# Performance work log

Measured on AMD Instinct MI355X. Metric: run time of the kernel, lower is better.

The kernel has to match this reference:

```python
import jax, jax.numpy as jnp
import numpy as np
from itertools import permutations

B, L, H, A, E, R, BS = 4, 1024, 768, 12, 32, 97, 64
P = E * (E - 1)  # ordered entity pairs per sample
HTS = np.array(list(permutations(range(E), 2)), dtype=np.int32)  # [P,2]


def setup_inputs() -> dict:
    key = jax.random.key(0)
    ks = jax.random.split(key, 8)
    return {
        "hidden_state": jax.random.normal(ks[0], (B, L, H), jnp.float32),
        "attention": jax.random.uniform(ks[1], (B, A, L, L), jnp.float32),
        "attention_mask": jnp.ones((B, L), jnp.float32),
        "head": jax.random.randint(ks[2], (B, E), 0, L, jnp.int32),
        "tail": jax.random.randint(ks[3], (B, E), 0, L, jnp.int32),
        # params (stored [in, out])
        "Wh": jax.random.normal(ks[4], (2 * H, H), jnp.float32) * 0.02,
        "bh": jnp.zeros((H,), jnp.float32),
        "Wt": jax.random.normal(ks[5], (2 * H, H), jnp.float32) * 0.02,
        "bt": jnp.zeros((H,), jnp.float32),
        "Wc": jax.random.normal(ks[6], (H * BS, R), jnp.float32) * 0.01,
        "bc": jnp.zeros((R,), jnp.float32),
    }


def reference(hidden_state, attention, attention_mask, head, tail, Wh, bh, Wt, bt, Wc, bc):
    attn = attention.mean(axis=1)  # [B,L,L]
    hts0 = jnp.asarray(HTS[:, 0])
    hts1 = jnp.asarray(HTS[:, 1])

    def per_sample(hid, at, hd, tl, am):
        ent_feat = (hid[hd] + hid[tl]) * 0.5   # [E,H]
        ent_attn = (at[hd] + at[tl]) * 0.5     # [E,L]
        head_f = ent_feat[hts0]                # [P,H]
        tail_f = ent_feat[hts1]                # [P,H]
        ht_attn = ent_attn[hts0] * ent_attn[hts1] * am  # [P,L]
        ht_attn = ht_attn / (ht_attn.sum(-1, keepdims=True) + 1e-20)
        ht_info = ht_attn @ hid                # [P,H]
        return (jnp.concatenate([head_f, ht_info], -1),
                jnp.concatenate([tail_f, ht_info], -1))

    all_h, all_t = jax.vmap(per_sample)(hidden_state, attn, head, tail, attention_mask)
    all_h = all_h.reshape(-1, 2 * H)  # [B*P, 2H]
    all_t = all_t.reshape(-1, 2 * H)
    h = jnp.tanh(all_h @ Wh + bh)     # [N,H]
    t = jnp.tanh(all_t @ Wt + bt)
    N = h.shape[0]
    # GroupLinear: block-diagonal outer product then linear
    outer = (h.reshape(N, H // BS, BS, 1) * t.reshape(N, H // BS, 1, BS)).reshape(N, H * BS)
    logits = outer @ Wc + bc          # [N,R]
    return logits
```

## Files before the change

kernel.cpp:

```cpp
#include <hip/hip_runtime.h>
#include <cstdint>
#include <cstddef>

#define BB 4
#define LL 1024
#define HH 768
#define AA 12
#define EE 32
#define PP 992
#define PPAD 1024
#define NROW (BB*PPAD)
#define NN (BB*PP)
#define RR 97
#define RP 112
#define GS2 16

typedef __attribute__((ext_vector_type(8))) _Float16 half8;
typedef __attribute__((ext_vector_type(4))) _Float16 half4v;
typedef __attribute__((ext_vector_type(2))) _Float16 half2v;
typedef __attribute__((ext_vector_type(4))) float floatx4;

union H8u { half8 v8; half2v v2[4]; };

#define WAITVM(N) asm volatile("s_waitcnt vmcnt(" #N ")" ::: "memory")

__device__ __forceinline__ void gl_lds16(const void* g, void* l) {
    __builtin_amdgcn_global_load_lds(
        (const __attribute__((address_space(1))) unsigned int*)g,
        (__attribute__((address_space(3))) unsigned int*)l, 16, 0, 0);
}

__device__ __forceinline__ void barrier_raw() {
    asm volatile("" ::: "memory");
    __builtin_amdgcn_s_barrier();
    __builtin_amdgcn_sched_barrier(0);
    asm volatile("" ::: "memory");
}

__device__ __forceinline__ int xswz96(int bid) {
    return (bid & 7) * 96 + (bid >> 3);
}

__device__ __forceinline__ void pair_decode(int p, int& i0, int& i1) {
    i0 = p / 31;
    int r = p - i0 * 31;
    i1 = r + (r >= i0 ? 1 : 0);
}

__device__ __forceinline__ float fast_tanh(float x) {
    float ax = fabsf(x);
    float t = __builtin_amdgcn_exp2f(ax * -2.885390082f);
    float r = (1.f - t) * __builtin_amdgcn_rcpf(1.f + t);
    return copysignf(r, x);
}

__global__ __launch_bounds__(256) void k_stage0(
        const float* __restrict__ hid, const float* __restrict__ att,
        const int* __restrict__ head, const int* __restrict__ tail,
        const float* __restrict__ Wh, const float* __restrict__ Wt,
        const float* __restrict__ Wc,
        _Float16* __restrict__ hidb, _Float16* __restrict__ Whf,
        _Float16* __restrict__ Wtf, _Float16* __restrict__ Wcp,
        float* __restrict__ ent_feat, float* __restrict__ ent_attn) {
    __shared__ float ldw[32][101];
    int bid = blockIdx.x, tid = threadIdx.x;
    if (bid < 1536) {
        int ksg = bid;
        int w = tid >> 6, lane = tid & 63;
        const float* src = Wc + (size_t)ksg * 32 * RR;
        #pragma unroll
        for (int rr = 0; rr < 8; ++rr) {
            int row = w * 8 + rr;
            ldw[row][lane] = src[(size_t)row * RR + lane];
            if (lane < 33) ldw[row][64 + lane] = src[(size_t)row * RR + 64 + lane];
        }
        __syncthreads();
        #pragma unroll
        for (int j = 0; j < 2; ++j) {
            int f = tid + j * 256;
            int rt = f >> 6, lf = f & 63;
            int c = rt * 16 + (lf & 15);
            int kb = (lf >> 4) * 8;
            _Float16 v[8];
            #pragma unroll
            for (int e = 0; e < 8; ++e)
                v[e] = (c < RR) ? (_Float16)ldw[kb + e][c] : (_Float16)0.f;
            *(half8*)(Wcp + ((size_t)ksg * 512 + f) * 8) = *(const half8*)v;
        }
    } else if (bid < 2112) {
        int which = (bid < 1824) ? 0 : 1;
        const float* src = (which ? Wt : Wh) + (size_t)HH * HH;
        _Float16* dst = which ? Wtf : Whf;
        int idx = (bid - (which ? 1824 : 1536)) * 256 + tid;
        int lane = idx & 63, f = idx >> 6;
        int ct = f % 48, ks = f / 48;
        int c = ct * 16 + (lane & 15);
        int kb = ks * 32 + (lane >> 4) * 8;
        _Float16 v[8];
        #pragma unroll
        for (int e = 0; e < 8; ++e)
            v[e] = (_Float16)src[(size_t)(kb + e) * HH + c];
        *(half8*)(dst + (size_t)idx * 8) = *(const half8*)v;
    } else if (bid < 3648) {
        int idx = (bid - 2112) * 256 + tid;
        const float* s = hid + (size_t)idx * 8;
        float4 a = *(const float4*)s;
        float4 b = *(const float4*)(s + 4);
        half8 v = { (_Float16)a.x, (_Float16)a.y, (_Float16)a.z, (_Float16)a.w,
                    (_Float16)b.x, (_Float16)b.y, (_Float16)b.z, (_Float16)b.w };
        *(half8*)(hidb + (size_t)idx * 8) = v;
    } else {
        int q = bid - 3648;
        int be = q >> 2, qt = q & 3;
        int b = be >> 5;
        int hd = head[be], tl = tail[be];
        const float* hrow = hid + ((size_t)b * LL + hd) * HH;
        const float* trow = hid + ((size_t)b * LL + tl) * HH;
        if (tid < 192) {
            int c = qt * 192 + tid;
            ent_feat[(size_t)be * HH + c] = 0.5f * (hrow[c] + trow[c]);
        }
        const float* abase = att + (size_t)b * AA * LL * LL;
        int ll = qt * 256 + tid;
        float s = 0.f;
        #pragma unroll
        for (int a = 0; a < AA; ++a) {
            const float* ar = abase + (size_t)a * LL * LL;
            s += ar[(size_t)hd * LL + ll] + ar[(size_t)tl * LL + ll];
        }
        ent_attn[(size_t)be * LL + ll] = s * (0.5f / AA);
    }
}

__global__ __launch_bounds__(256) void k_stage1(
        const float* __restrict__ ent_attn, const float* __restrict__ am,
        const float* __restrict__ ent_feat,
        const float* __restrict__ Wh, const float* __restrict__ bh,
        const float* __restrict__ Wt, const float* __restrict__ bt,
        _Float16* __restrict__ pairw, float* __restrict__ Fht) {
    __shared__ float fs[EE][68];
    __shared__ float ws_[64][68];
    int tid = threadIdx.x;
    if (blockIdx.x < 1024) {
        int lane = tid & 63, w = tid >> 6;
        int prow = blockIdx.x * 4 + w;
        int b = prow >> 10, p = prow & 1023;
        _Float16* dst = pairw + (size_t)prow * LL;
        if (p >= PP) {
            #pragma unroll
            for (int c = 0; c < 4; ++c) {
                half4v z = {};
                *(half4v*)(dst + c * 256 + lane * 4) = z;
            }
            return;
        }
        int i0, i1; pair_decode(p, i0, i1);
        const float* e0  = ent_attn + ((size_t)b * EE + i0) * LL;
        const float* e1  = ent_attn + ((size_t)b * EE + i1) * LL;
        const float* amr = am + (size_t)b * LL;
        float wv[16];
        float s = 0.f;
        #pragma unroll
        for (int c = 0; c < 4; ++c) {
            int o = c * 256 + lane * 4;
            float4 a = *(const float4*)(e0 + o);
            float4 d = *(const float4*)(e1 + o);
            float4 m = *(const float4*)(amr + o);
            wv[c*4+0] = a.x * d.x * m.x; wv[c*4+1] = a.y * d.y * m.y;
            wv[c*4+2] = a.z * d.z * m.z; wv[c*4+3] = a.w * d.w * m.w;
            s += wv[c*4+0] + wv[c*4+1] + wv[c*4+2] + wv[c*4+3];
        }
        #pragma unroll
        for (int off = 32; off > 0; off >>= 1) s += __shfl_down(s, off, 64);
        float tot = __shfl(s, 0, 64);
        float inv = 1.0f / (tot + 1e-20f);
        #pragma unroll
        for (int c = 0; c < 4; ++c) {
            half4v o4 = { (_Float16)(wv[c*4+0] * inv), (_Float16)(wv[c*4+1] * inv),
                          (_Float16)(wv[c*4+2] * inv), (_Float16)(wv[c*4+3] * inv) };
            *(half4v*)(dst + c * 256 + lane * 4) = o4;
        }
    } else {
        int q = blockIdx.x - 1024;
        int ct = q % 12, b = (q / 12) % BB, mat = q / 48;
        const float* W    = mat ? Wt : Wh;
        const float* bias = mat ? bt : bh;
        int e = tid >> 3, cg = tid & 7;
        float acc[8] = {};
        for (int k0 = 0; k0 < HH; k0 += 64) {
            __syncthreads();
            #pragma unroll
            for (int it = 0; it < 2; ++it) {
                int idx = tid + it * 256;
                int ee = idx >> 4, kk = (idx & 15) * 4;
                *(float4*)(&fs[ee][kk]) =
                    *(const float4*)(ent_feat + ((size_t)b * EE + ee) * HH + k0 + kk);
            }
            #pragma unroll
            for (int it = 0; it < 4; ++it) {
                int idx = tid + it * 256;
                int kk = idx >> 4, cc = (idx & 15) * 4;
                *(float4*)(&ws_[kk][cc]) =
                    *(const float4*)(W + (size_t)(k0 + kk) * HH + ct * 64 + cc);
            }
            __syncthreads();
            #pragma unroll
            for (int kk = 0; kk < 64; ++kk) {
                float f = fs[e][kk];
                float4 w0 = *(const float4*)(&ws_[kk][cg * 8]);
                float4 w1 = *(const float4*)(&ws_[kk][cg * 8 + 4]);
                acc[0] += f * w0.x; acc[1] += f * w0.y; acc[2] += f * w0.z; acc[3] += f * w0.w;
                acc[4] += f * w1.x; acc[5] += f * w1.y; acc[6] += f * w1.z; acc[7] += f * w1.w;
            }
        }
        int cbase = ct * 64 + cg * 8;
        float* dst = Fht + (((size_t)mat * BB + b) * EE + e) * HH + cbase;
        #pragma unroll
        for (int j = 0; j < 8; ++j) dst[j] = acc[j] + bias[cbase + j];
    }
}

__global__ __launch_bounds__(128) void k_vgemm(
        const _Float16* __restrict__ hidb,
        const _Float16* __restrict__ Whf, const _Float16* __restrict__ Wtf,
        _Float16* __restrict__ Vhf, _Float16* __restrict__ Vtf) {
    int bid = xswz96(blockIdx.x);
    int cb = bid >> 6, mI = bid & 63;
    int ct0 = cb * 4;
    __shared__ __align__(16) _Float16 Bs[4][4096];
    int tid = threadIdx.x, lane = tid & 63, wid = tid >> 6;
    int r0 = wid * 32 + (lane & 15);
    int kg8 = (lane >> 4) * 8;

    const _Float16* A0 = hidb + (size_t)(mI * 64 + r0) * HH + kg8;
    const _Float16* A1 = A0 + 16 * HH;
    const char* WhB = (const char*)Whf + (size_t)ct0 * 1024;
    const char* WtB = (const char*)Wtf + (size_t)ct0 * 1024;
    char* LB = (char*)&Bs[0][0];
    int lo = wid * 2048 + lane * 16;
    int ld = wid * 2048;

    #pragma unroll
    for (int j = 0; j < 2; ++j) {
        gl_lds16(WhB + j * 1024 + lo, LB + j * 1024 + ld);
        gl_lds16(WtB + j * 1024 + lo, LB + 4096 + j * 1024 + ld);
    }
    half8 a0c = *(const half8*)A0;
    half8 a1c = *(const half8*)A1;
    {
        const char* hs = WhB + 49152;
        const char* ts = WtB + 49152;
        #pragma unroll
        for (int j = 0; j < 2; ++j) {
            gl_lds16(hs + j * 1024 + lo, LB + 8192 + j * 1024 + ld);
            gl_lds16(ts + j * 1024 + lo, LB + 8192 + 4096 + j * 1024 + ld);
        }
    }
    floatx4 aH[2][4] = {}, aT[2][4] = {};
    half8 a0n = a0c, a1n = a1c;
    for (int ks = 0; ks < 24; ++ks) {
        int buf = ks & 3;
        if (ks < 23) {
            a0n = *(const half8*)(A0 + (ks + 1) * 32);
            a1n = *(const half8*)(A1 + (ks + 1) * 32);
        }
        if (ks < 22) {
            const char* hs = WhB + (size_t)(ks + 2) * 49152;
            const char* ts = WtB + (size_t)(ks + 2) * 49152;
            char* lb = LB + ((ks + 2) & 3) * 8192;
            #pragma unroll
            for (int j = 0; j < 2; ++j) {
                gl_lds16(hs + j * 1024 + lo, lb + j * 1024 + ld);
                gl_lds16(ts + j * 1024 + lo, lb + 4096 + j * 1024 + ld);
            }
            WAITVM(12);
        } else if (ks == 22) { WAITVM(8); } else { WAITVM(2); }
        barrier_raw();
        const half8* bp = (const half8*)(LB + buf * 8192) + lane;
        __builtin_amdgcn_s_setprio(1);
        #pragma unroll
        for (int ct = 0; ct < 4; ++ct) {
            half8 bvh = bp[ct * 64];
            half8 bvt = bp[256 + ct * 64];
            aH[0][ct] = __builtin_amdgcn_mfma_f32_16x16x32_f16(a0c, bvh, aH[0][ct], 0, 0, 0);
            aH[1][ct] = __builtin_amdgcn_mfma_f32_16x16x32_f16(a1c, bvh, aH[1][ct], 0, 0, 0);
            aT[0][ct] = __builtin_amdgcn_mfma_f32_16x16x32_f16(a0c, bvt, aT[0][ct], 0, 0, 0);
            aT[1][ct] = __builtin_amdgcn_mfma_f32_16x16x32_f16(a1c, bvt, aT[1][ct], 0, 0, 0);
        }
        __builtin_amdgcn_s_setprio(0);
        a0c = a0n; a1c = a1n;
    }
    int b = mI >> 4;
    int kspB = (mI & 15) * 2 + wid;
    int u = lane >> 4, rb = lane & 15;
    int estart = (u & 1) * 4;
    size_t bofs = (size_t)b * 786432;
    #pragma unroll
    for (int rs = 0; rs < 2; ++rs) {
        int laneL = (rs * 2 + (u >> 1)) * 16 + rb;
        #pragma unroll
        for (int ct = 0; ct < 4; ++ct) {
            size_t base = bofs + ((size_t)(kspB * 48 + ct0 + ct) * 64 + laneL) * 8 + estart;
            half4v hv = { (_Float16)aH[rs][ct][0], (_Float16)aH[rs][ct][1],
                          (_Float16)aH[rs][ct][2], (_Float16)aH[rs][ct][3] };
            half4v tv = { (_Float16)aT[rs][ct][0], (_Float16)aT[rs][ct][1],
                          (_Float16)aT[rs][ct][2], (_Float16)aT[rs][ct][3] };
            *(half4v*)(Vhf + base) = hv;
            *(half4v*)(Vtf + base) = tv;
        }
    }
}

__global__ __launch_bounds__(128) void k_proj_mfma(
        const _Float16* __restrict__ pairw,
        const _Float16* __restrict__ Vhf, const _Float16* __restrict__ Vtf,
        const float* __restrict__ Fht,
        _Float16* __restrict__ hb, _Float16* __restrict__ tb) {
    int bid = xswz96(blockIdx.x);
    int bc = bid >> 4, mI = bid & 15;
    int b = bc / 12, cb = bc - b * 12;
    int ct0 = cb * 4;
    __shared__ __align__(16) _Float16 Bs[4][4096];
    int tid = threadIdx.x, lane = tid & 63, wid = tid >> 6;
    int r0 = wid * 32 + (lane & 15);
    int kg8 = (lane >> 4) * 8;

    const _Float16* A0 = pairw + (size_t)(b * PPAD + mI * 64 + r0) * LL + kg8;
    const _Float16* A1 = A0 + 16 * LL;
    const char* VhB = (const char*)(Vhf + (size_t)b * 786432) + (size_t)ct0 * 1024;
    const char* VtB = (const char*)(Vtf + (size_t)b * 786432) + (size_t)ct0 * 1024;
    char* LB = (char*)&Bs[0][0];
    int lo = wid * 2048 + lane * 16;
    int ld = wid * 2048;

    #pragma unroll
    for (int j = 0; j < 2; ++j) {
        gl_lds16(VhB + j * 1024 + lo, LB + j * 1024 + ld);
        gl_lds16(VtB + j * 1024 + lo, LB + 4096 + j * 1024 + ld);
    }
    half8 a0c = *(const half8*)A0;
    half8 a1c = *(const half8*)A1;
    {
        const char* hs = VhB + 49152;
        const char* ts = VtB + 49152;
        #pragma unroll
        for (int j = 0; j < 2; ++j) {
            gl_lds16(hs + j * 1024 + lo, LB + 8192 + j * 1024 + ld);
            gl_lds16(ts + j * 1024 + lo, LB + 8192 + 4096 + j * 1024 + ld);
        }
    }
    floatx4 aH[2][4] = {}, aT4[2][4] = {};
    half8 a0n = a0c, a1n = a1c;
    for (int ks = 0; ks < 32; ++ks) {
        int buf = ks & 3;
        if (ks < 31) {
            a0n = *(const half8*)(A0 + (ks + 1) * 32);
            a1n = *(const half8*)(A1 + (ks + 1) * 32);
        }
        if (ks < 30) {
            const char* hs = VhB + (size_t)(ks + 2) * 49152;
            const char* ts = VtB + (size_t)(ks + 2) * 49152;
            char* lb = LB + ((ks + 2) & 3) * 8192;
            #pragma unroll
            for (int j = 0; j < 2; ++j) {
                gl_lds16(hs + j * 1024 + lo, lb + j * 1024 + ld);
                gl_lds16(ts + j * 1024 + lo, lb + 4096 + j * 1024 + ld);
            }
            WAITVM(12);
        } else if (ks == 30) { WAITVM(8); } else { WAITVM(2); }
        barrier_raw();
        const half8* bp = (const half8*)(LB + buf * 8192) + lane;
        __builtin_amdgcn_s_setprio(1);
        #pragma unroll
        for (int ct = 0; ct < 4; ++ct) {
            half8 bvh = bp[ct * 64];
            half8 bvt = bp[256 + ct * 64];
            aH[0][ct]  = __builtin_amdgcn_mfma_f32_16x16x32_f16(a0c, bvh, aH[0][ct], 0, 0, 0);
            aH[1][ct]  = __builtin_amdgcn_mfma_f32_16x16x32_f16(a1c, bvh, aH[1][ct], 0, 0, 0);
            aT4[0][ct] = __builtin_amdgcn_mfma_f32_16x16x32_f16(a0c, bvt, aT4[0][ct], 0, 0, 0);
            aT4[1][ct] = __builtin_amdgcn_mfma_f32_16x16x32_f16(a1c, bvt, aT4[1][ct], 0, 0, 0);
        }
        __builtin_amdgcn_s_setprio(0);
        a0c = a0n; a1c = a1n;
    }
    const float* FhB = Fht + (size_t)b * EE * HH;
    const float* FtB = Fht + (size_t)(BB + b) * EE * HH;
    int u = lane >> 4, rb = lane & 15;
    #pragma unroll
    for (int rs = 0; rs < 2; ++rs) {
        int pb = mI * 64 + wid * 32 + rs * 16 + u * 4;
        int i0a[4], i1a[4];
        #pragma unroll
        for (int q = 0; q < 4; ++q) {
            int p = pb + q;
            if (p < PP) pair_decode(p, i0a[q], i1a[q]);
            else { i0a[q] = -1; i1a[q] = -1; }
        }
        #pragma unroll
        for (int ct = 0; ct < 4; ++ct) {
            int c = (ct0 + ct) * 16 + rb;
            #pragma unroll
            for (int q = 0; q < 4; ++q) {
                size_t row = (size_t)b * PPAD + pb + q;
                _Float16 hv = (_Float16)0.f, tv = (_Float16)0.f;
                if (i0a[q] >= 0) {
                    hv = (_Float16)fast_tanh(aH[rs][ct][q]  + FhB[(size_t)i0a[q] * HH + c]);
                    tv = (_Float16)fast_tanh(aT4[rs][ct][q] + FtB[(size_t)i1a[q] * HH + c]);
                }
                hb[row * HH + c] = hv;
                tb[row * HH + c] = tv;
            }
        }
    }
}

__global__ __launch_bounds__(256) void k_logits_mfma(
        const _Float16* __restrict__ hb, const _Float16* __restrict__ tb,
        const _Float16* __restrict__ Wcp, _Float16* __restrict__ part) {
    int bid = blockIdx.x;
    int gs = (bid & 7) * 2 + ((bid >> 3) & 1);
    int nb = bid >> 4;
    int n0 = nb * 128;
    int hcol0 = gs * 48;
    int g0 = (3 * gs) >> 2;
    int tcol0 = g0 * 64;
    __shared__ __align__(16) _Float16 hT[6][128][8];
    __shared__ __align__(16) _Float16 tT[16][128][8];
    __shared__ __align__(16) _Float16 Bs[4][4096];
    int tid = threadIdx.x, lane = tid & 63, wid = tid >> 6;

    #pragma unroll
    for (int it = 0; it < 3; ++it) {
        int idx = tid + it * 256;
        int ch = idx >> 7, row = idx & 127;
        *(half8*)&hT[ch][row][0] =
            *(const half8*)(hb + (size_t)(n0 + row) * HH + hcol0 + ch * 8);
    }
    int nch = (HH - tcol0) >> 3;
    #pragma unroll
    for (int it = 0; it < 8; ++it) {
        int idx = tid + it * 256;
        int ch = idx >> 7, row = idx & 127;
        if (ch < nch)
            *(half8*)&tT[ch][row][0] =
                *(const half8*)(tb + (size_t)(n0 + row) * HH + tcol0 + ch * 8);
    }
    __syncthreads();

    const char* WcB = (const char*)Wcp + (size_t)gs * 96 * 8192;
    char* LB = (char*)&Bs[0][0];
    int lo = wid * 2048 + lane * 16;
    int ld = wid * 2048;
    #pragma unroll
    for (int s = 0; s < 2; ++s) {
        const char* sp = WcB + (size_t)s * 8192;
        char* lb = LB + s * 8192;
        gl_lds16(sp + lo, lb + ld);
        gl_lds16(sp + 1024 + lo, lb + 1024 + ld);
    }
    int r0 = wid * 32 + (lane & 15);
    int kgrp = lane >> 4;
    floatx4 acc[2][7] = {};

    for (int ks = 0; ks < 96; ++ks) {
        int buf = ks & 3;
        int ksg = gs * 96 + ks;
        int g = ksg >> 7;
        int kin = ksg & 127;
        int i = kin >> 1, jh = kin & 1;
        int hloc = g * 64 + i - hcol0;
        int chT = ((g * 64 + jh * 32 - tcol0) >> 3) + kgrp;
        _Float16 h0 = hT[hloc >> 3][r0][hloc & 7];
        _Float16 h1 = hT[hloc >> 3][r0 + 16][hloc & 7];
        H8u t0u, t1u, a0, a1;
        t0u.v8 = *(const half8*)&tT[chT][r0][0];
        t1u.v8 = *(const half8*)&tT[chT][r0 + 16][0];
        half2v h02 = { h0, h0 }, h12 = { h1, h1 };
        #pragma unroll
        for (int q = 0; q < 4; ++q) {
            a0.v2[q] = h02 * t0u.v2[q];
            a1.v2[q] = h12 * t1u.v2[q];
        }
        if (ks < 94) {
            const char* sp = WcB + (size_t)(ks + 2) * 8192;
            char* lb = LB + ((ks + 2) & 3) * 8192;
            gl_lds16(sp + lo, lb + ld);
            gl_lds16(sp + 1024 + lo, lb + 1024 + ld);
            WAITVM(4);
        } else if (ks == 94) { WAITVM(2); } else { WAITVM(0); }
        barrier_raw();
        const half8* bp = (const half8*)(LB + buf * 8192) + lane;
        __builtin_amdgcn_s_setprio(1);
        #pragma unroll
        for (int rt = 0; rt < 7; ++rt) {
            half8 bv = bp[rt * 64];
            acc[0][rt] = __builtin_amdgcn_mfma_f32_16x16x32_f16(a0.v8, bv, acc[0][rt], 0, 0, 0);
            acc[1][rt] = __builtin_amdgcn_mfma_f32_16x16x32_f16(a1.v8, bv, acc[1][rt], 0, 0, 0);
        }
        __builtin_amdgcn_s_setprio(0);
    }
    int rb = lane & 15, u = lane >> 4;
    #pragma unroll
    for (int rs = 0; rs < 2; ++rs) {
        int nbase = n0 + wid * 32 + rs * 16 + u * 4;
        #pragma unroll
        for (int rt = 0; rt < 7; ++rt)
            #pragma unroll
            for (int q = 0; q < 4; ++q)
                part[((size_t)gs * NROW + nbase + q) * RP + rt * 16 + rb] =
                    (_Float16)acc[rs][rt][q];
    }
}

__global__ __launch_bounds__(256) void k_reduce(
        const _Float16* __restrict__ part, const float* __restrict__ bc,
        float* __restrict__ out) {
    int idx = blockIdx.x * 256 + threadIdx.x;
    if (idx >= NN * RR) return;
    int n = idx / RR;
    int r = idx - n * RR;
    int b = n / PP, p = n - b * PP;
    size_t rowp = (size_t)b * PPAD + p;
    float s = bc[r];
    #pragma unroll
    for (int g = 0; g < GS2; ++g)
        s += (float)part[((size_t)g * NROW + rowp) * RP + r];
    out[idx] = s;
}

extern "C" void kernel_launch(void* const* d_in, const int* in_sizes, int n_in,
                              void* d_out, int out_size, void* d_ws, size_t ws_size,
                              hipStream_t stream) {
    const float* hid  = (const float*)d_in[0];
    const float* att  = (const float*)d_in[1];
    const float* am   = (const float*)d_in[2];
    const int*   head = (const int*)d_in[3];
    const int*   tail = (const int*)d_in[4];
    const float* Wh   = (const float*)d_in[5];
    const float* bh   = (const float*)d_in[6];
    const float* Wt   = (const float*)d_in[7];
    const float* bt   = (const float*)d_in[8];
    const float* Wc   = (const float*)d_in[9];
    const float* bc   = (const float*)d_in[10];
    float* out = (float*)d_out;

    char* w = (char*)d_ws;
    _Float16* Wcp = (_Float16*)w;  w += (size_t)1536 * 512 * 8 * 2;
    _Float16* Vhf = (_Float16*)w;  w += (size_t)BB * 786432 * 2;
    _Float16* Vtf = (_Float16*)w;  w += (size_t)BB * 786432 * 2;
    _Float16* hbv = (_Float16*)w;  w += (size_t)NROW * HH * 2;
    _Float16* tbv = (_Float16*)w;  w += (size_t)NROW * HH * 2;
    float* Fht      = (float*)w;   w += (size_t)2 * BB * EE * HH * 4;
    float* ent_feat = (float*)w;   w += (size_t)BB * EE * HH * 4;
    float* ent_attn = (float*)w;   w += (size_t)BB * EE * LL * 4;
    char* alias = w;
    _Float16* hidb  = (_Float16*)alias;
    _Float16* Whf   = (_Float16*)(alias + 6291456);
    _Float16* Wtf   = (_Float16*)(alias + 6291456 + 1179648);
    _Float16* pairw = (_Float16*)(alias + 6291456 + 2 * 1179648);
    _Float16* part  = (_Float16*)alias;

    k_stage0<<<4160, 256, 0, stream>>>(hid, att, head, tail, Wh, Wt, Wc,
                                       hidb, Whf, Wtf, Wcp, ent_feat, ent_attn);
    k_stage1<<<1120, 256, 0, stream>>>(ent_attn, am, ent_feat, Wh, bh, Wt, bt, pairw, Fht);
    k_vgemm<<<768, 128, 0, stream>>>(hidb, Whf, Wtf, Vhf, Vtf);
    k_proj_mfma<<<768, 128, 0, stream>>>(pairw, Vhf, Vtf, Fht, hbv, tbv);
    k_logits_mfma<<<512, 256, 0, stream>>>(hbv, tbv, Wcp, part);
    k_reduce<<<1504, 256, 0, stream>>>(part, bc, out);
}
```

Before: 146.9 us.

## Fuse entity-feature GEMM into stage0 and store proj outputs chunk-major for async LDS loads

The Fh/Ft entity-projection GEMM moves from stage1 into stage0. It computes the entity features on the fly from hidden rows via head/tail indices, so the ent_feat buffer and its dependency on stage0 are gone and stage1 only builds the pair weights. The proj kernel now writes h/t activations in an 8-column-chunk-major layout. This lets the logits kernel stage its h/t tiles with direct global-to-LDS 16-byte loads instead of strided per-row vector loads. Costs are scattered 2-byte stores in the proj epilogue and extra LDS in the larger stage0 kernel, which may lower its occupancy.

```diff
diff --git a/kernel.cpp b/kernel.cpp
--- a/kernel.cpp
+++ b/kernel.cpp
@@ -57,12 +57,16 @@
 __global__ __launch_bounds__(256) void k_stage0(
         const float* __restrict__ hid, const float* __restrict__ att,
         const int* __restrict__ head, const int* __restrict__ tail,
-        const float* __restrict__ Wh, const float* __restrict__ Wt,
+        const float* __restrict__ Wh, const float* __restrict__ bh,
+        const float* __restrict__ Wt, const float* __restrict__ bt,
         const float* __restrict__ Wc,
         _Float16* __restrict__ hidb, _Float16* __restrict__ Whf,
         _Float16* __restrict__ Wtf, _Float16* __restrict__ Wcp,
-        float* __restrict__ ent_feat, float* __restrict__ ent_attn) {
+        float* __restrict__ ent_attn, float* __restrict__ Fht) {
     __shared__ float ldw[32][101];
+    __shared__ float fs[EE][68];
+    __shared__ float ws_[64][68];
+    __shared__ int hds[EE], tls[EE];
     int bid = blockIdx.x, tid = threadIdx.x;
     if (bid < 1536) {
         int ksg = bid;
@@ -109,17 +113,11 @@
         half8 v = { (_Float16)a.x, (_Float16)a.y, (_Float16)a.z, (_Float16)a.w,
                     (_Float16)b.x, (_Float16)b.y, (_Float16)b.z, (_Float16)b.w };
         *(half8*)(hidb + (size_t)idx * 8) = v;
-    } else {
+    } else if (bid < 4160) {
         int q = bid - 3648;
         int be = q >> 2, qt = q & 3;
         int b = be >> 5;
         int hd = head[be], tl = tail[be];
-        const float* hrow = hid + ((size_t)b * LL + hd) * HH;
-        const float* trow = hid + ((size_t)b * LL + tl) * HH;
-        if (tid < 192) {
-            int c = qt * 192 + tid;
-            ent_feat[(size_t)be * HH + c] = 0.5f * (hrow[c] + trow[c]);
-        }
         const float* abase = att + (size_t)b * AA * LL * LL;
         int ll = qt * 256 + tid;
         float s = 0.f;
@@ -129,62 +127,16 @@
             s += ar[(size_t)hd * LL + ll] + ar[(size_t)tl * LL + ll];
         }
         ent_attn[(size_t)be * LL + ll] = s * (0.5f / AA);
-    }
-}
-
-__global__ __launch_bounds__(256) void k_stage1(
-        const float* __restrict__ ent_attn, const float* __restrict__ am,
-        const float* __restrict__ ent_feat,
-        const float* __restrict__ Wh, const float* __restrict__ bh,
-        const float* __restrict__ Wt, const float* __restrict__ bt,
-        _Float16* __restrict__ pairw, float* __restrict__ Fht) {
-    __shared__ float fs[EE][68];
-    __shared__ float ws_[64][68];
-    int tid = threadIdx.x;
-    if (blockIdx.x < 1024) {
-        int lane = tid & 63, w = tid >> 6;
-        int prow = blockIdx.x * 4 + w;
-        int b = prow >> 10, p = prow & 1023;
-        _Float16* dst = pairw + (size_t)prow * LL;
-        if (p >= PP) {
-            #pragma unroll
-            for (int c = 0; c < 4; ++c) {
-                half4v z = {};
-                *(half4v*)(dst + c * 256 + lane * 4) = z;
-            }
-            return;
-        }
-        int i0, i1; pair_decode(p, i0, i1);
-        const float* e0  = ent_attn + ((size_t)b * EE + i0) * LL;
-        const float* e1  = ent_attn + ((size_t)b * EE + i1) * LL;
-        const float* amr = am + (size_t)b * LL;
-        float wv[16];
-        float s = 0.f;
-        #pragma unroll
-        for (int c = 0; c < 4; ++c) {
-            int o = c * 256 + lane * 4;
-            float4 a = *(const float4*)(e0 + o);
-            float4 d = *(const float4*)(e1 + o);
-            float4 m = *(const float4*)(amr + o);
-            wv[c*4+0] = a.x * d.x * m.x; wv[c*4+1] = a.y * d.y * m.y;
-            wv[c*4+2] = a.z * d.z * m.z; wv[c*4+3] = a.w * d.w * m.w;
-            s += wv[c*4+0] + wv[c*4+1] + wv[c*4+2] + wv[c*4+3];
-        }
-        #pragma unroll
-        for (int off = 32; off > 0; off >>= 1) s += __shfl_down(s, off, 64);
-        float tot = __shfl(s, 0, 64);
-        float inv = 1.0f / (tot + 1e-20f);
-        #pragma unroll
-        for (int c = 0; c < 4; ++c) {
-            half4v o4 = { (_Float16)(wv[c*4+0] * inv), (_Float16)(wv[c*4+1] * inv),
-                          (_Float16)(wv[c*4+2] * inv), (_Float16)(wv[c*4+3] * inv) };
-            *(half4v*)(dst + c * 256 + lane * 4) = o4;
-        }
     } else {
-        int q = blockIdx.x - 1024;
+        int q = bid - 4160;
         int ct = q % 12, b = (q / 12) % BB, mat = q / 48;
         const float* W    = mat ? Wt : Wh;
         const float* bias = mat ? bt : bh;
+        if (tid < EE) {
+            hds[tid] = head[b * EE + tid];
+            tls[tid] = tail[b * EE + tid];
+        }
+        __syncthreads();
         int e = tid >> 3, cg = tid & 7;
         float acc[8] = {};
         for (int k0 = 0; k0 < HH; k0 += 64) {
@@ -193,8 +145,11 @@
             for (int it = 0; it < 2; ++it) {
                 int idx = tid + it * 256;
                 int ee = idx >> 4, kk = (idx & 15) * 4;
-                *(float4*)(&fs[ee][kk]) =
-                    *(const float4*)(ent_feat + ((size_t)b * EE + ee) * HH + k0 + kk);
+                float4 a = *(const float4*)(hid + ((size_t)b * LL + hds[ee]) * HH + k0 + kk);
+                float4 c = *(const float4*)(hid + ((size_t)b * LL + tls[ee]) * HH + k0 + kk);
+                float4 m = { 0.5f * (a.x + c.x), 0.5f * (a.y + c.y),
+                             0.5f * (a.z + c.z), 0.5f * (a.w + c.w) };
+                *(float4*)(&fs[ee][kk]) = m;
             }
             #pragma unroll
             for (int it = 0; it < 4; ++it) {
@@ -217,6 +172,50 @@
         float* dst = Fht + (((size_t)mat * BB + b) * EE + e) * HH + cbase;
         #pragma unroll
         for (int j = 0; j < 8; ++j) dst[j] = acc[j] + bias[cbase + j];
+    }
+}
+
+__global__ __launch_bounds__(256) void k_stage1(
+        const float* __restrict__ ent_attn, const float* __restrict__ am,
+        _Float16* __restrict__ pairw) {
+    int tid = threadIdx.x;
+    int lane = tid & 63, w = tid >> 6;
+    int prow = blockIdx.x * 4 + w;
+    int b = prow >> 10, p = prow & 1023;
+    _Float16* dst = pairw + (size_t)prow * LL;
+    if (p >= PP) {
+        #pragma unroll
+        for (int c = 0; c < 4; ++c) {
+            half4v z = {};
+            *(half4v*)(dst + c * 256 + lane * 4) = z;
+        }
+        return;
+    }
+    int i0, i1; pair_decode(p, i0, i1);
+    const float* e0  = ent_attn + ((size_t)b * EE + i0) * LL;
+    const float* e1  = ent_attn + ((size_t)b * EE + i1) * LL;
+    const float* amr = am + (size_t)b * LL;
+    float wv[16];
+    float s = 0.f;
+    #pragma unroll
+    for (int c = 0; c < 4; ++c) {
+        int o = c * 256 + lane * 4;
+        float4 a = *(const float4*)(e0 + o);
+        float4 d = *(const float4*)(e1 + o);
+        float4 m = *(const float4*)(amr + o);
+        wv[c*4+0] = a.x * d.x * m.x; wv[c*4+1] = a.y * d.y * m.y;
+        wv[c*4+2] = a.z * d.z * m.z; wv[c*4+3] = a.w * d.w * m.w;
+        s += wv[c*4+0] + wv[c*4+1] + wv[c*4+2] + wv[c*4+3];
+    }
+    #pragma unroll
+    for (int off = 32; off > 0; off >>= 1) s += __shfl_down(s, off, 64);
+    float tot = __shfl(s, 0, 64);
+    float inv = 1.0f / (tot + 1e-20f);
+    #pragma unroll
+    for (int c = 0; c < 4; ++c) {
+        half4v o4 = { (_Float16)(wv[c*4+0] * inv), (_Float16)(wv[c*4+1] * inv),
+                      (_Float16)(wv[c*4+2] * inv), (_Float16)(wv[c*4+3] * inv) };
+        *(half4v*)(dst + c * 256 + lane * 4) = o4;
     }
 }
 
@@ -315,7 +314,7 @@
         const _Float16* __restrict__ pairw,
         const _Float16* __restrict__ Vhf, const _Float16* __restrict__ Vtf,
         const float* __restrict__ Fht,
-        _Float16* __restrict__ hb, _Float16* __restrict__ tb) {
+        _Float16* __restrict__ hb2, _Float16* __restrict__ tb2) {
     int bid = xswz96(blockIdx.x);
     int bc = bid >> 4, mI = bid & 15;
     int b = bc / 12, cb = bc - b * 12;
@@ -399,6 +398,7 @@
         #pragma unroll
         for (int ct = 0; ct < 4; ++ct) {
             int c = (ct0 + ct) * 16 + rb;
+            int c8 = c >> 3, ce = c & 7;
             #pragma unroll
             for (int q = 0; q < 4; ++q) {
                 size_t row = (size_t)b * PPAD + pb + q;
@@ -407,43 +407,42 @@
                     hv = (_Float16)fast_tanh(aH[rs][ct][q]  + FhB[(size_t)i0a[q] * HH + c]);
                     tv = (_Float16)fast_tanh(aT4[rs][ct][q] + FtB[(size_t)i1a[q] * HH + c]);
                 }
-                hb[row * HH + c] = hv;
-                tb[row * HH + c] = tv;
+                hb2[((size_t)c8 * NROW + row) * 8 + ce] = hv;
+                tb2[((size_t)c8 * NROW + row) * 8 + ce] = tv;
             }
         }
     }
 }
 
 __global__ __launch_bounds__(256) void k_logits_mfma(
-        const _Float16* __restrict__ hb, const _Float16* __restrict__ tb,
+        const _Float16* __restrict__ hb2, const _Float16* __restrict__ tb2,
         const _Float16* __restrict__ Wcp, _Float16* __restrict__ part) {
     int bid = blockIdx.x;
     int gs = (bid & 7) * 2 + ((bid >> 3) & 1);
     int nb = bid >> 4;
     int n0 = nb * 128;
-    int hcol0 = gs * 48;
     int g0 = (3 * gs) >> 2;
-    int tcol0 = g0 * 64;
+    int hch0 = gs * 6;
+    int tch0 = g0 * 8;
     __shared__ __align__(16) _Float16 hT[6][128][8];
     __shared__ __align__(16) _Float16 tT[16][128][8];
     __shared__ __align__(16) _Float16 Bs[4][4096];
     int tid = threadIdx.x, lane = tid & 63, wid = tid >> 6;
 
-    #pragma unroll
-    for (int it = 0; it < 3; ++it) {
-        int idx = tid + it * 256;
-        int ch = idx >> 7, row = idx & 127;
-        *(half8*)&hT[ch][row][0] =
-            *(const half8*)(hb + (size_t)(n0 + row) * HH + hcol0 + ch * 8);
-    }
-    int nch = (HH - tcol0) >> 3;
-    #pragma unroll
-    for (int it = 0; it < 8; ++it) {
-        int idx = tid + it * 256;
-        int ch = idx >> 7, row = idx & 127;
-        if (ch < nch)
-            *(half8*)&tT[ch][row][0] =
-                *(const half8*)(tb + (size_t)(n0 + row) * HH + tcol0 + ch * 8);
+    for (int hc = wid; hc < 12; hc += 4) {
+        int ch = hc >> 1, half = hc & 1;
+        const char* src = (const char*)(hb2 +
+            ((size_t)(hch0 + ch) * NROW + n0 + half * 64) * 8) + lane * 16;
+        gl_lds16(src, (char*)&hT[ch][half * 64][0]);
+    }
+    int nchT = 96 - tch0; if (nchT > 16) nchT = 16;
+    for (int hc = wid; hc < 32; hc += 4) {
+        int ch = hc >> 1, half = hc & 1;
+        if (ch < nchT) {
+            const char* src = (const char*)(tb2 +
+                ((size_t)(tch0 + ch) * NROW + n0 + half * 64) * 8) + lane * 16;
+            gl_lds16(src, (char*)&tT[ch][half * 64][0]);
+        }
     }
     __syncthreads();
 
@@ -460,6 +459,7 @@
     }
     int r0 = wid * 32 + (lane & 15);
     int kgrp = lane >> 4;
+    int hcol0 = gs * 48, tcol0 = g0 * 64;
     floatx4 acc[2][7] = {};
 
     for (int ks = 0; ks < 96; ++ks) {
@@ -548,10 +548,9 @@
     _Float16* Wcp = (_Float16*)w;  w += (size_t)1536 * 512 * 8 * 2;
     _Float16* Vhf = (_Float16*)w;  w += (size_t)BB * 786432 * 2;
     _Float16* Vtf = (_Float16*)w;  w += (size_t)BB * 786432 * 2;
-    _Float16* hbv = (_Float16*)w;  w += (size_t)NROW * HH * 2;
-    _Float16* tbv = (_Float16*)w;  w += (size_t)NROW * HH * 2;
+    _Float16* hb2 = (_Float16*)w;  w += (size_t)96 * NROW * 8 * 2;
+    _Float16* tb2 = (_Float16*)w;  w += (size_t)96 * NROW * 8 * 2;
     float* Fht      = (float*)w;   w += (size_t)2 * BB * EE * HH * 4;
-    float* ent_feat = (float*)w;   w += (size_t)BB * EE * HH * 4;
     float* ent_attn = (float*)w;   w += (size_t)BB * EE * LL * 4;
     char* alias = w;
     _Float16* hidb  = (_Float16*)alias;
@@ -560,11 +559,11 @@
     _Float16* pairw = (_Float16*)(alias + 6291456 + 2 * 1179648);
     _Float16* part  = (_Float16*)alias;
 
-    k_stage0<<<4160, 256, 0, stream>>>(hid, att, head, tail, Wh, Wt, Wc,
-                                       hidb, Whf, Wtf, Wcp, ent_feat, ent_attn);
-    k_stage1<<<1120, 256, 0, stream>>>(ent_attn, am, ent_feat, Wh, bh, Wt, bt, pairw, Fht);
+    k_stage0<<<4256, 256, 0, stream>>>(hid, att, head, tail, Wh, bh, Wt, bt, Wc,
+                                       hidb, Whf, Wtf, Wcp, ent_attn, Fht);
+    k_stage1<<<1024, 256, 0, stream>>>(ent_attn, am, pairw);
     k_vgemm<<<768, 128, 0, stream>>>(hidb, Whf, Wtf, Vhf, Vtf);
-    k_proj_mfma<<<768, 128, 0, stream>>>(pairw, Vhf, Vtf, Fht, hbv, tbv);
-    k_logits_mfma<<<512, 256, 0, stream>>>(hbv, tbv, Wcp, part);
+    k_proj_mfma<<<768, 128, 0, stream>>>(pairw, Vhf, Vtf, Fht, hb2, tb2);
+    k_logits_mfma<<<512, 256, 0, stream>>>(hb2, tb2, Wcp, part);
     k_reduce<<<1504, 256, 0, stream>>>(part, bc, out);
 }
```

New measurement: 167.2 us. +13.9%, slower.

## Compute entity-feature projection with fp16 MFMA from hidb instead of fp32 FMA

Applied to the files above, without the earlier changes.

The small entity-feature projection (ent_feat @ Wh/Wt top half) moves from an fp32 shared-memory FMA loop to fp16 MFMA 16x16x32 instructions. Entity features are now formed on the fly from the fp16 hidden copy, so the ent_feat buffer and its stage-0 work go away. Stage 0 gains extra blocks that pack the first half of Wh/Wt into an MFMA-friendly fp16 layout. This trades fp32 precision for fp16 in the projection and adds weight-conversion traffic to stage 0.

```diff
diff --git a/kernel.cpp b/kernel.cpp
--- a/kernel.cpp
+++ b/kernel.cpp
@@ -60,8 +60,9 @@
         const float* __restrict__ Wh, const float* __restrict__ Wt,
         const float* __restrict__ Wc,
         _Float16* __restrict__ hidb, _Float16* __restrict__ Whf,
-        _Float16* __restrict__ Wtf, _Float16* __restrict__ Wcp,
-        float* __restrict__ ent_feat, float* __restrict__ ent_attn) {
+        _Float16* __restrict__ Wtf, _Float16* __restrict__ W1hf,
+        _Float16* __restrict__ W1tf, _Float16* __restrict__ Wcp,
+        float* __restrict__ ent_attn) {
     __shared__ float ldw[32][101];
     int bid = blockIdx.x, tid = threadIdx.x;
     if (bid < 1536) {
@@ -109,17 +110,11 @@
         half8 v = { (_Float16)a.x, (_Float16)a.y, (_Float16)a.z, (_Float16)a.w,
                     (_Float16)b.x, (_Float16)b.y, (_Float16)b.z, (_Float16)b.w };
         *(half8*)(hidb + (size_t)idx * 8) = v;
-    } else {
+    } else if (bid < 4160) {
         int q = bid - 3648;
         int be = q >> 2, qt = q & 3;
         int b = be >> 5;
         int hd = head[be], tl = tail[be];
-        const float* hrow = hid + ((size_t)b * LL + hd) * HH;
-        const float* trow = hid + ((size_t)b * LL + tl) * HH;
-        if (tid < 192) {
-            int c = qt * 192 + tid;
-            ent_feat[(size_t)be * HH + c] = 0.5f * (hrow[c] + trow[c]);
-        }
         const float* abase = att + (size_t)b * AA * LL * LL;
         int ll = qt * 256 + tid;
         float s = 0.f;
@@ -129,17 +124,30 @@
             s += ar[(size_t)hd * LL + ll] + ar[(size_t)tl * LL + ll];
         }
         ent_attn[(size_t)be * LL + ll] = s * (0.5f / AA);
+    } else {
+        int which = (bid < 4448) ? 0 : 1;
+        const float* src = which ? Wt : Wh;
+        _Float16* dst = which ? W1tf : W1hf;
+        int idx = (bid - (which ? 4448 : 4160)) * 256 + tid;
+        int lane = idx & 63, f = idx >> 6;
+        int ct = f % 48, ks = f / 48;
+        int c = ct * 16 + (lane & 15);
+        int kb = ks * 32 + (lane >> 4) * 8;
+        _Float16 v[8];
+        #pragma unroll
+        for (int e = 0; e < 8; ++e)
+            v[e] = (_Float16)src[(size_t)(kb + e) * HH + c];
+        *(half8*)(dst + (size_t)idx * 8) = *(const half8*)v;
     }
 }
 
 __global__ __launch_bounds__(256) void k_stage1(
         const float* __restrict__ ent_attn, const float* __restrict__ am,
-        const float* __restrict__ ent_feat,
-        const float* __restrict__ Wh, const float* __restrict__ bh,
-        const float* __restrict__ Wt, const float* __restrict__ bt,
+        const int* __restrict__ head, const int* __restrict__ tail,
+        const _Float16* __restrict__ hidb,
+        const _Float16* __restrict__ W1hf, const _Float16* __restrict__ W1tf,
+        const float* __restrict__ bh, const float* __restrict__ bt,
         _Float16* __restrict__ pairw, float* __restrict__ Fht) {
-    __shared__ float fs[EE][68];
-    __shared__ float ws_[64][68];
     int tid = threadIdx.x;
     if (blockIdx.x < 1024) {
         int lane = tid & 63, w = tid >> 6;
@@ -183,40 +191,38 @@
     } else {
         int q = blockIdx.x - 1024;
         int ct = q % 12, b = (q / 12) % BB, mat = q / 48;
-        const float* W    = mat ? Wt : Wh;
+        const _Float16* Wf = mat ? W1tf : W1hf;
         const float* bias = mat ? bt : bh;
-        int e = tid >> 3, cg = tid & 7;
-        float acc[8] = {};
-        for (int k0 = 0; k0 < HH; k0 += 64) {
-            __syncthreads();
-            #pragma unroll
-            for (int it = 0; it < 2; ++it) {
-                int idx = tid + it * 256;
-                int ee = idx >> 4, kk = (idx & 15) * 4;
-                *(float4*)(&fs[ee][kk]) =
-                    *(const float4*)(ent_feat + ((size_t)b * EE + ee) * HH + k0 + kk);
-            }
-            #pragma unroll
-            for (int it = 0; it < 4; ++it) {
-                int idx = tid + it * 256;
-                int kk = idx >> 4, cc = (idx & 15) * 4;
-                *(float4*)(&ws_[kk][cc]) =
-                    *(const float4*)(W + (size_t)(k0 + kk) * HH + ct * 64 + cc);
-            }
-            __syncthreads();
-            #pragma unroll
-            for (int kk = 0; kk < 64; ++kk) {
-                float f = fs[e][kk];
-                float4 w0 = *(const float4*)(&ws_[kk][cg * 8]);
-                float4 w1 = *(const float4*)(&ws_[kk][cg * 8 + 4]);
-                acc[0] += f * w0.x; acc[1] += f * w0.y; acc[2] += f * w0.z; acc[3] += f * w0.w;
-                acc[4] += f * w1.x; acc[5] += f * w1.y; acc[6] += f * w1.z; acc[7] += f * w1.w;
-            }
-        }
-        int cbase = ct * 64 + cg * 8;
-        float* dst = Fht + (((size_t)mat * BB + b) * EE + e) * HH + cbase;
-        #pragma unroll
-        for (int j = 0; j < 8; ++j) dst[j] = acc[j] + bias[cbase + j];
+        int lane = tid & 63, w = tid >> 6;
+        int row = (w & 1) * 16 + (lane & 15);
+        int k8 = (lane >> 4) * 8;
+        int hd = head[b * EE + row], tl = tail[b * EE + row];
+        const _Float16* Ah = hidb + ((size_t)b * LL + hd) * HH + k8;
+        const _Float16* At = hidb + ((size_t)b * LL + tl) * HH + k8;
+        int ctG0 = ct * 4 + (w >> 1) * 2;
+        const half8* B0 = (const half8*)Wf + (size_t)ctG0 * 64 + lane;
+        floatx4 acc[2] = {};
+        half2v hlf = { (_Float16)0.5f, (_Float16)0.5f };
+        for (int ks = 0; ks < 24; ++ks) {
+            H8u a_, b_, av;
+            a_.v8 = *(const half8*)(Ah + ks * 32);
+            b_.v8 = *(const half8*)(At + ks * 32);
+            #pragma unroll
+            for (int qq = 0; qq < 4; ++qq) av.v2[qq] = (a_.v2[qq] + b_.v2[qq]) * hlf;
+            const half8* Bk = B0 + (size_t)ks * 48 * 64;
+            acc[0] = __builtin_amdgcn_mfma_f32_16x16x32_f16(av.v8, Bk[0], acc[0], 0, 0, 0);
+            acc[1] = __builtin_amdgcn_mfma_f32_16x16x32_f16(av.v8, Bk[64], acc[1], 0, 0, 0);
+        }
+        int rb = lane & 15, u = lane >> 4;
+        #pragma unroll
+        for (int cc = 0; cc < 2; ++cc) {
+            int c = (ctG0 + cc) * 16 + rb;
+            float bi = bias[c];
+            float* dst = Fht + (((size_t)mat * BB + b) * EE + (w & 1) * 16 + u * 4) * HH + c;
+            #pragma unroll
+            for (int qq = 0; qq < 4; ++qq)
+                dst[(size_t)qq * HH] = acc[cc][qq] + bi;
+        }
     }
 }
 
@@ -551,18 +557,20 @@
     _Float16* hbv = (_Float16*)w;  w += (size_t)NROW * HH * 2;
     _Float16* tbv = (_Float16*)w;  w += (size_t)NROW * HH * 2;
     float* Fht      = (float*)w;   w += (size_t)2 * BB * EE * HH * 4;
-    float* ent_feat = (float*)w;   w += (size_t)BB * EE * HH * 4;
     float* ent_attn = (float*)w;   w += (size_t)BB * EE * LL * 4;
     char* alias = w;
     _Float16* hidb  = (_Float16*)alias;
     _Float16* Whf   = (_Float16*)(alias + 6291456);
     _Float16* Wtf   = (_Float16*)(alias + 6291456 + 1179648);
     _Float16* pairw = (_Float16*)(alias + 6291456 + 2 * 1179648);
+    _Float16* W1hf  = (_Float16*)(alias + 6291456 + 2 * 1179648 + 8388608);
+    _Float16* W1tf  = (_Float16*)(alias + 6291456 + 3 * 1179648 + 8388608);
     _Float16* part  = (_Float16*)alias;
 
-    k_stage0<<<4160, 256, 0, stream>>>(hid, att, head, tail, Wh, Wt, Wc,
-                                       hidb, Whf, Wtf, Wcp, ent_feat, ent_attn);
-    k_stage1<<<1120, 256, 0, stream>>>(ent_attn, am, ent_feat, Wh, bh, Wt, bt, pairw, Fht);
+    k_stage0<<<4736, 256, 0, stream>>>(hid, att, head, tail, Wh, Wt, Wc,
+                                       hidb, Whf, Wtf, W1hf, W1tf, Wcp, ent_attn);
+    k_stage1<<<1120, 256, 0, stream>>>(ent_attn, am, head, tail, hidb,
+                                       W1hf, W1tf, bh, bt, pairw, Fht);
     k_vgemm<<<768, 128, 0, stream>>>(hidb, Whf, Wtf, Vhf, Vtf);
     k_proj_mfma<<<768, 128, 0, stream>>>(pairw, Vhf, Vtf, Fht, hbv, tbv);
     k_logits_mfma<<<512, 256, 0, stream>>>(hbv, tbv, Wcp, part);
```

New measurement: 132.6 us, median of 2. 1.11x faster.
